# Optimization experiments

Measured on AMD Instinct MI355X. Metric: run time of the kernel, lower is better.

Reference implementation:

```python
import jax, jax.numpy as jnp
import numpy as np

B = 16384          # batch
F = 64             # number of feature columns (tables)
L = 10             # pooled lookups per feature (bag size)
E = 16             # embedding dim
V = 1_000_000      # hashed vocab size (shared table)
D = F * E          # concat width = 1024
EPS = 1e-5


def setup_inputs() -> dict:
    key = jax.random.key(0)
    ks = jax.random.split(key, 9)
    idx = jax.random.randint(ks[0], (B, F, L), 0, V, dtype=jnp.int64)
    # NormalTensorInitializer(var=0.01) -> std 0.1
    emb = jax.random.normal(ks[1], (V, E), dtype=jnp.float32) * 0.1
    W1 = jax.random.normal(ks[2], (D, 1024), dtype=jnp.float32) / np.sqrt(D).astype(np.float32)
    b1 = jnp.zeros((1024,), jnp.float32)
    W2 = jax.random.normal(ks[3], (1024, 512), dtype=jnp.float32) / np.sqrt(1024).astype(np.float32)
    b2 = jnp.zeros((512,), jnp.float32)
    W3 = jax.random.normal(ks[4], (512, 1), dtype=jnp.float32) / np.sqrt(512).astype(np.float32)
    b3 = jnp.zeros((1,), jnp.float32)
    return {"idx": idx, "emb": emb, "W1": W1, "b1": b1,
            "W2": W2, "b2": b2, "W3": W3, "b3": b3}


def reference(idx, emb, W1, b1, W2, b2, W3, b3):
    # EmbeddingSumConcat: gather [B,F,L,E], sum-pool over bag dim, concat features
    pooled = jnp.take(emb, idx, axis=0).sum(axis=2)          # [B, F, E]
    x = pooled.reshape(B, D)                                  # [B, F*E]
    # ms.nn.Normalization: per-feature batch standardization
    mu = x.mean(axis=0, keepdims=True)
    var = x.var(axis=0, keepdims=True)
    x = (x - mu) * jax.lax.rsqrt(var + EPS)
    # Dense tower 1024 -> 1024 -> 512 -> 1, sigmoid
    h = jax.nn.relu(x @ W1 + b1)
    h = jax.nn.relu(h @ W2 + b2)
    out = jax.nn.sigmoid(h @ W3 + b3)                         # [B, 1]
    return out
```

## Files before the change

### kernel.cpp

```cpp
#include <hip/hip_runtime.h>
#include <hip/hip_bf16.h>
#include <math.h>

typedef __attribute__((ext_vector_type(8))) short  short8;
typedef __attribute__((ext_vector_type(4))) float  f32x4;
typedef __attribute__((ext_vector_type(4))) unsigned short u16x4;
typedef __attribute__((ext_vector_type(8))) unsigned short u16x8;

#define BATCH 16384
#define NF    64
#define BAGL  10
#define ED    16
#define DW    1024
#define VOCAB 1000000

static __device__ __forceinline__ unsigned short f2bf(float f) {
    unsigned int u = __builtin_bit_cast(unsigned int, f);
    unsigned int r = (u + 0x7fffu + ((u >> 16) & 1u)) >> 16;
    return (unsigned short)r;
}
static __device__ __forceinline__ float bf2f(unsigned short h) {
    unsigned int u = ((unsigned int)h) << 16;
    return __builtin_bit_cast(float, u);
}

__global__ __launch_bounds__(256) void pool_kernel(const int* __restrict__ idx,
                                                   const float* __restrict__ emb,
                                                   unsigned short* __restrict__ xb) {
    const int gid = blockIdx.x * 256 + threadIdx.x;
    const int bag = gid >> 2;
    const int q   = gid & 3;
    const int* ip = idx + (long long)bag * BAGL;

    int v[BAGL];
#pragma unroll
    for (int l = 0; l < BAGL; ++l) v[l] = ip[l];
    f32x4 e[BAGL];
#pragma unroll
    for (int l = 0; l < BAGL; ++l)
        e[l] = *(const f32x4*)(emb + (((long long)v[l]) << 4) + (q << 2));

    f32x4 s01 = e[0] + e[1], s23 = e[2] + e[3], s45 = e[4] + e[5],
          s67 = e[6] + e[7], s89 = e[8] + e[9];
    f32x4 acc = ((s01 + s23) + (s45 + s67)) + s89;

    u16x4 o;
#pragma unroll
    for (int j = 0; j < 4; ++j) o[j] = f2bf(acc[j]);
    *(u16x4*)(xb + (((long long)bag) << 4) + (q << 2)) = o;
}

__global__ __launch_bounds__(256) void stats_kernel(const unsigned short* __restrict__ xb,
                                                    float* __restrict__ ssum,
                                                    float* __restrict__ ssq) {
    const int t = threadIdx.x;
    const long long r0 = (long long)blockIdx.x * 128;
    float s[4] = {0, 0, 0, 0}, q[4] = {0, 0, 0, 0};
    for (int r = 0; r < 128; ++r) {
        const u16x4 v = *(const u16x4*)(xb + (r0 + r) * DW + t * 4);
#pragma unroll
        for (int j = 0; j < 4; ++j) { float f = bf2f(v[j]); s[j] += f; q[j] += f * f; }
    }
#pragma unroll
    for (int j = 0; j < 4; ++j) {
        atomicAdd(&ssum[t * 4 + j], s[j]);
        atomicAdd(&ssq [t * 4 + j], q[j]);
    }
}

__global__ void finalize_stats(const float* __restrict__ ssum, const float* __restrict__ ssq,
                               float* __restrict__ mean, float* __restrict__ rsig,
                               float* __restrict__ murs) {
    const int c = blockIdx.x * 256 + threadIdx.x;
    const float m = ssum[c] * (1.0f / (float)BATCH);
    const float v = ssq[c] * (1.0f / (float)BATCH) - m * m;
    const float r = rsqrtf(v + 1e-5f);
    mean[c] = m; rsig[c] = r; murs[c] = m * r;
}

template <int SCALE>
__global__ __launch_bounds__(256) void transpose_f32_bf16(const float* __restrict__ src,
                                                          unsigned short* __restrict__ dst,
                                                          int R, int C,
                                                          const float* __restrict__ rs) {
    __shared__ float tile[32][33];
    const int tx = threadIdx.x & 31, ty = threadIdx.x >> 5;
    const int bx = blockIdx.x, by = blockIdx.y;
#pragma unroll
    for (int i = 0; i < 4; ++i) {
        const int r = by * 32 + ty + i * 8, c = bx * 32 + tx;
        float v = src[(long long)r * C + c];
        if (SCALE) v *= rs[r];
        tile[ty + i * 8][tx] = v;
    }
    __syncthreads();
#pragma unroll
    for (int i = 0; i < 4; ++i) {
        const int oc = bx * 32 + ty + i * 8;
        dst[(long long)oc * R + by * 32 + tx] = f2bf(tile[tx][ty + i * 8]);
    }
}

__global__ __launch_bounds__(256) void b1fold_kernel(const float* __restrict__ W1,
                                                     const float* __restrict__ murs,
                                                     float* __restrict__ b1n) {
    const int n = blockIdx.x * 256 + threadIdx.x;
    const int k0 = blockIdx.y * 128;
    float acc = 0.f;
#pragma unroll 4
    for (int k = 0; k < 128; ++k)
        acc += murs[k0 + k] * W1[(long long)(k0 + k) * 1024 + n];
    atomicAdd(&b1n[n], -acc);
}

__global__ __launch_bounds__(512, 2) void gemm1_256(const unsigned short* __restrict__ A,
                                                    const unsigned short* __restrict__ Bt,
                                                    const float* __restrict__ bias,
                                                    const float* __restrict__ bias2,
                                                    unsigned short* __restrict__ C,
                                                    int M, int N, int K) {
    __shared__ __align__(16) unsigned short As[2][256 * 64];
    __shared__ __align__(16) unsigned short Bs[2][256 * 64];
    const int tid = threadIdx.x;
    const int w = tid >> 6, l = tid & 63;
    const int wr = w >> 2, wc = w & 3;
    const int l15 = l & 15, l4 = l >> 4;
    const int blk = blockIdx.x, xcd = blk & 7, jj = blk >> 3;
    const int bm = xcd * 8 + (jj >> 2), bn = jj & 3;

    f32x4 acc[8][4] = {};
    const long long a_base = (long long)bm * 256 * K;
    const long long b_base = (long long)bn * 256 * K;
    const int NT = K >> 6;

#define G1_STAGE(buf, kt)                                                       \
  {                                                                             \
    const int k0s = (kt) * 64;                                                  \
    _Pragma("unroll")                                                           \
    for (int g = 0; g < 4; ++g) {                                               \
      const int cid = g * 512 + tid;                                            \
      const int rr = cid >> 3, pos = cid & 7;                                   \
      const int csrc = (pos ^ (rr & 7)) << 3;                                   \
      __builtin_amdgcn_global_load_lds(                                         \
        (const __attribute__((address_space(1))) void*)(A + a_base + (long long)rr * K + k0s + csrc), \
        (__attribute__((address_space(3))) void*)(&As[buf][cid * 8]), 16, 0, 0);\
      __builtin_amdgcn_global_load_lds(                                         \
        (const __attribute__((address_space(1))) void*)(Bt + b_base + (long long)rr * K + k0s + csrc), \
        (__attribute__((address_space(3))) void*)(&Bs[buf][cid * 8]), 16, 0, 0);\
    }                                                                           \
  }

    G1_STAGE(0, 0)
    G1_STAGE(1, 1)
    asm volatile("s_waitcnt vmcnt(8)" ::: "memory");
    __builtin_amdgcn_sched_barrier(0);
    __builtin_amdgcn_s_barrier();

    for (int t = 0; t < NT; ++t) {
        const unsigned short* Ap = As[t & 1];
        const unsigned short* Bp = Bs[t & 1];
        short8 a[8], b[4];

        {
            const int swz = ((0 * 4 + l4) ^ (l15 & 7)) << 3;
#pragma unroll
            for (int m = 0; m < 8; ++m)
                a[m] = *(const short8*)(Ap + (wr * 128 + m * 16 + l15) * 64 + swz);
#pragma unroll
            for (int n = 0; n < 4; ++n)
                b[n] = *(const short8*)(Bp + (wc * 64 + n * 16 + l15) * 64 + swz);
        }
        asm volatile("s_waitcnt lgkmcnt(0)" ::: "memory");
        __builtin_amdgcn_sched_barrier(0);
        __builtin_amdgcn_s_setprio(1);
#pragma unroll
        for (int m = 0; m < 8; ++m)
#pragma unroll
            for (int n = 0; n < 4; ++n)
                acc[m][n] = __builtin_amdgcn_mfma_f32_16x16x32_bf16(a[m], b[n], acc[m][n], 0, 0, 0);
        __builtin_amdgcn_s_setprio(0);

        {
            const int swz = ((1 * 4 + l4) ^ (l15 & 7)) << 3;
#pragma unroll
            for (int m = 0; m < 8; ++m)
                a[m] = *(const short8*)(Ap + (wr * 128 + m * 16 + l15) * 64 + swz);
#pragma unroll
            for (int n = 0; n < 4; ++n)
                b[n] = *(const short8*)(Bp + (wc * 64 + n * 16 + l15) * 64 + swz);
        }
        asm volatile("s_waitcnt lgkmcnt(0)" ::: "memory");
        __builtin_amdgcn_sched_barrier(0);
        __builtin_amdgcn_s_barrier();
        if (t + 2 < NT) { G1_STAGE((t & 1), t + 2) }
        __builtin_amdgcn_s_setprio(1);
#pragma unroll
        for (int m = 0; m < 8; ++m)
#pragma unroll
            for (int n = 0; n < 4; ++n)
                acc[m][n] = __builtin_amdgcn_mfma_f32_16x16x32_bf16(a[m], b[n], acc[m][n], 0, 0, 0);
        __builtin_amdgcn_s_setprio(0);
        if (t + 1 < NT) {
            if (t + 2 < NT) { asm volatile("s_waitcnt vmcnt(8)" ::: "memory"); }
            else            { asm volatile("s_waitcnt vmcnt(0)" ::: "memory"); }
            __builtin_amdgcn_sched_barrier(0);
            __builtin_amdgcn_s_barrier();
        }
    }
#undef G1_STAGE

#pragma unroll
    for (int m = 0; m < 8; ++m) {
        const int grow_base = bm * 256 + wr * 128 + m * 16 + l4 * 4;
#pragma unroll
        for (int n = 0; n < 4; ++n) {
            const int gcol = bn * 256 + wc * 64 + n * 16 + l15;
            const float bv = bias[gcol] + bias2[gcol];
#pragma unroll
            for (int j2 = 0; j2 < 4; ++j2) {
                float v = fmaxf(acc[m][n][j2] + bv, 0.f);
                C[(long long)(grow_base + j2) * N + gcol] = f2bf(v);
            }
        }
    }
}

#define GEMM_STAGE(dstA, dstB, kt)                                              \
  {                                                                             \
    const int k0s = (kt) * 64;                                                  \
    _Pragma("unroll")                                                           \
    for (int g = 0; g < 4; ++g) {                                               \
      const int cid = g * 256 + tid;                                            \
      const int rr = cid >> 3, pos = cid & 7;                                   \
      const int csrc = (pos ^ (rr & 7)) << 3;                                   \
      __builtin_amdgcn_global_load_lds(                                         \
        (const __attribute__((address_space(1))) void*)(A + a_base + (long long)rr * K + k0s + csrc), \
        (__attribute__((address_space(3))) void*)(&(dstA)[cid * 8]), 16, 0, 0); \
      __builtin_amdgcn_global_load_lds(                                         \
        (const __attribute__((address_space(1))) void*)(Bt + b_base + (long long)rr * K + k0s + csrc), \
        (__attribute__((address_space(3))) void*)(&(dstB)[cid * 8]), 16, 0, 0); \
    }                                                                           \
  }

__global__ __launch_bounds__(256, 2) void gemm2_fused(const unsigned short* __restrict__ A,
                                                      const unsigned short* __restrict__ Bt,
                                                      const float* __restrict__ bias,
                                                      const float* __restrict__ W3,
                                                      float* __restrict__ logits,
                                                      int M, int N, int K, int NBN) {
    __shared__ __align__(16) unsigned short As[2][128 * 64];
    __shared__ __align__(16) unsigned short Bs[2][128 * 64];
    const int tid = threadIdx.x;
    const int w = tid >> 6, l = tid & 63;
    const int wr = w >> 1, wc = w & 1;
    const int l15 = l & 15, l4 = l >> 4;
    const int blk = blockIdx.x, xcd = blk & 7, j = blk >> 3;
    const int bm = xcd * 16 + j / NBN, bn = j % NBN;

    f32x4 acc[4][4] = {};
    const long long a_base = (long long)bm * 128 * K;
    const long long b_base = (long long)bn * 128 * K;
    const int NT = K >> 6;

    GEMM_STAGE(As[0], Bs[0], 0)
    GEMM_STAGE(As[1], Bs[1], 1)
    asm volatile("s_waitcnt vmcnt(8)" ::: "memory");
    __builtin_amdgcn_sched_barrier(0);
    __builtin_amdgcn_s_barrier();
    for (int t = 0; t < NT; ++t) {
        const unsigned short* Ap = As[t & 1];
        const unsigned short* Bp = Bs[t & 1];
        short8 a[2][4], b[2][4];
#pragma unroll
        for (int kk = 0; kk < 2; ++kk) {
            const int swz = ((kk * 4 + l4) ^ (l15 & 7)) << 3;
#pragma unroll
            for (int m = 0; m < 4; ++m)
                a[kk][m] = *(const short8*)(Ap + (wr * 64 + m * 16 + l15) * 64 + swz);
#pragma unroll
            for (int n = 0; n < 4; ++n)
                b[kk][n] = *(const short8*)(Bp + (wc * 64 + n * 16 + l15) * 64 + swz);
        }
        asm volatile("s_waitcnt lgkmcnt(0)" ::: "memory");
        __builtin_amdgcn_sched_barrier(0);
        __builtin_amdgcn_s_barrier();
        if (t + 2 < NT) { GEMM_STAGE(As[t & 1], Bs[t & 1], t + 2) }
        __builtin_amdgcn_s_setprio(1);
#pragma unroll
        for (int kk = 0; kk < 2; ++kk)
#pragma unroll
            for (int m = 0; m < 4; ++m)
#pragma unroll
                for (int n = 0; n < 4; ++n)
                    acc[m][n] = __builtin_amdgcn_mfma_f32_16x16x32_bf16(a[kk][m], b[kk][n], acc[m][n], 0, 0, 0);
        __builtin_amdgcn_s_setprio(0);
        if (t + 1 < NT) {
            if (t + 2 < NT) { asm volatile("s_waitcnt vmcnt(8)" ::: "memory"); }
            else            { asm volatile("s_waitcnt vmcnt(0)" ::: "memory"); }
            __builtin_amdgcn_sched_barrier(0);
            __builtin_amdgcn_s_barrier();
        }
    }

#pragma unroll
    for (int m = 0; m < 4; ++m) {
        float part[4] = {0.f, 0.f, 0.f, 0.f};
#pragma unroll
        for (int n = 0; n < 4; ++n) {
            const int gcol = bn * 128 + wc * 64 + n * 16 + l15;
            const float bv = bias[gcol];
            const float w3 = W3[gcol];
#pragma unroll
            for (int j2 = 0; j2 < 4; ++j2) {
                float v = fmaxf(acc[m][n][j2] + bv, 0.f);
                part[j2] += v * w3;
            }
        }
#pragma unroll
        for (int off = 1; off < 16; off <<= 1)
#pragma unroll
            for (int j2 = 0; j2 < 4; ++j2) part[j2] += __shfl_xor(part[j2], off, 64);
        if (l15 == 0) {
            const int grow = bm * 128 + wr * 64 + m * 16 + l4 * 4;
#pragma unroll
            for (int j2 = 0; j2 < 4; ++j2) atomicAdd(&logits[grow + j2], part[j2]);
        }
    }
}

__global__ __launch_bounds__(256) void sigmoid_kernel(const float* __restrict__ logits,
                                                      const float* __restrict__ b3,
                                                      float* __restrict__ out) {
    const int i = blockIdx.x * 256 + threadIdx.x;
    out[i] = 1.0f / (1.0f + expf(-(logits[i] + b3[0])));
}

extern "C" void kernel_launch(void* const* d_in, const int* in_sizes, int n_in,
                              void* d_out, int out_size, void* d_ws, size_t ws_size,
                              hipStream_t stream) {
    const int*   idx = (const int*)d_in[0];
    const float* emb = (const float*)d_in[1];
    const float* W1  = (const float*)d_in[2];
    const float* b1  = (const float*)d_in[3];
    const float* W2  = (const float*)d_in[4];
    const float* b2  = (const float*)d_in[5];
    const float* W3  = (const float*)d_in[6];
    const float* b3  = (const float*)d_in[7];
    float* out = (float*)d_out;

    char* ws = (char*)d_ws;
    unsigned short* xb   = (unsigned short*)ws; ws += (size_t)BATCH * DW * 2;
    unsigned short* h1   = (unsigned short*)ws; ws += (size_t)BATCH * DW * 2;
    unsigned short* w1t  = (unsigned short*)ws; ws += (size_t)1024 * 1024 * 2;
    unsigned short* w2t  = (unsigned short*)ws; ws += (size_t)512 * 1024 * 2;
    float* ssum   = (float*)ws; ws += 4096;
    float* ssq    = (float*)ws; ws += 4096;
    float* b1n    = (float*)ws; ws += 4096;
    float* logits = (float*)ws; ws += (size_t)BATCH * 4;
    float* mean   = (float*)ws; ws += 4096;
    float* rsig   = (float*)ws; ws += 4096;
    float* murs   = (float*)ws; ws += 4096;

    hipMemsetAsync(ssum, 0, 4096 * 3 + (size_t)BATCH * 4, stream);

    pool_kernel<<<(BATCH * NF * 4) / 256, 256, 0, stream>>>(idx, emb, xb);
    stats_kernel<<<BATCH / 128, 256, 0, stream>>>(xb, ssum, ssq);
    finalize_stats<<<4, 256, 0, stream>>>(ssum, ssq, mean, rsig, murs);

    transpose_f32_bf16<1><<<dim3(32, 32), 256, 0, stream>>>(W1, w1t, 1024, 1024, rsig);
    b1fold_kernel<<<dim3(4, 8), 256, 0, stream>>>(W1, murs, b1n);
    transpose_f32_bf16<0><<<dim3(16, 32), 256, 0, stream>>>(W2, w2t, 1024, 512, nullptr);

    gemm1_256<<<(BATCH / 256) * (1024 / 256), 512, 0, stream>>>(
        xb, w1t, b1, b1n, h1, BATCH, 1024, 1024);
    gemm2_fused<<<(BATCH / 128) * (512 / 128), 256, 0, stream>>>(
        h1, w2t, b2, W3, logits, BATCH, 512, 1024, 512 / 128);

    sigmoid_kernel<<<BATCH / 256, 256, 0, stream>>>(logits, b3, out);
}
```

Before: 296.9 us.

## Fuse stats finalize into weight prep, merge transposes, asm embedding loads

Drops the finalize_stats kernel by computing rsqrt of the variance inline in the weight transpose and bias-fold kernels. Merges the W1 and W2 transposes into one launch using a z-dimension. Doubles the number of stats blocks so each covers fewer rows. Rewrites the embedding gather with inline-asm global_load_dwordx4 using 32-bit offsets against a scalar base, which removes 64-bit address math but assumes every offset fits in 32 bits.

```diff
diff --git a/kernel.cpp b/kernel.cpp
--- a/kernel.cpp
+++ b/kernel.cpp
@@ -31,17 +31,24 @@
     const int bag = gid >> 2;
     const int q   = gid & 3;
     const int* ip = idx + (long long)bag * BAGL;
-
-    int v[BAGL];
-#pragma unroll
-    for (int l = 0; l < BAGL; ++l) v[l] = ip[l];
-    f32x4 e[BAGL];
-#pragma unroll
-    for (int l = 0; l < BAGL; ++l)
-        e[l] = *(const f32x4*)(emb + (((long long)v[l]) << 4) + (q << 2));
-
-    f32x4 s01 = e[0] + e[1], s23 = e[2] + e[3], s45 = e[4] + e[5],
-          s67 = e[6] + e[7], s89 = e[8] + e[9];
+    const unsigned qb = (unsigned)(q << 4);
+
+    unsigned o0 = ((unsigned)ip[0] << 6) + qb, o1 = ((unsigned)ip[1] << 6) + qb,
+             o2 = ((unsigned)ip[2] << 6) + qb, o3 = ((unsigned)ip[3] << 6) + qb,
+             o4 = ((unsigned)ip[4] << 6) + qb, o5 = ((unsigned)ip[5] << 6) + qb,
+             o6 = ((unsigned)ip[6] << 6) + qb, o7 = ((unsigned)ip[7] << 6) + qb,
+             o8 = ((unsigned)ip[8] << 6) + qb, o9 = ((unsigned)ip[9] << 6) + qb;
+
+    f32x4 e0, e1, e2, e3, e4, e5, e6, e7, e8, e9;
+#define GLD(e, o) asm volatile("global_load_dwordx4 %0, %1, %2" \
+                               : "=v"(e) : "v"(o), "s"(emb))
+    GLD(e0, o0); GLD(e1, o1); GLD(e2, o2); GLD(e3, o3); GLD(e4, o4);
+    GLD(e5, o5); GLD(e6, o6); GLD(e7, o7); GLD(e8, o8); GLD(e9, o9);
+#undef GLD
+    asm volatile("s_waitcnt vmcnt(0)" ::: "memory");
+    __builtin_amdgcn_sched_barrier(0);
+
+    f32x4 s01 = e0 + e1, s23 = e2 + e3, s45 = e4 + e5, s67 = e6 + e7, s89 = e8 + e9;
     f32x4 acc = ((s01 + s23) + (s45 + s67)) + s89;
 
     u16x4 o;
@@ -54,9 +61,9 @@
                                                     float* __restrict__ ssum,
                                                     float* __restrict__ ssq) {
     const int t = threadIdx.x;
-    const long long r0 = (long long)blockIdx.x * 128;
+    const long long r0 = (long long)blockIdx.x * 64;
     float s[4] = {0, 0, 0, 0}, q[4] = {0, 0, 0, 0};
-    for (int r = 0; r < 128; ++r) {
+    for (int r = 0; r < 64; ++r) {
         const u16x4 v = *(const u16x4*)(xb + (r0 + r) * DW + t * 4);
 #pragma unroll
         for (int j = 0; j < 4; ++j) { float f = bf2f(v[j]); s[j] += f; q[j] += f * f; }
@@ -68,48 +75,57 @@
     }
 }
 
-__global__ void finalize_stats(const float* __restrict__ ssum, const float* __restrict__ ssq,
-                               float* __restrict__ mean, float* __restrict__ rsig,
-                               float* __restrict__ murs) {
-    const int c = blockIdx.x * 256 + threadIdx.x;
+static __device__ __forceinline__ float rsig_of(const float* ssum, const float* ssq, int c) {
     const float m = ssum[c] * (1.0f / (float)BATCH);
     const float v = ssq[c] * (1.0f / (float)BATCH) - m * m;
-    const float r = rsqrtf(v + 1e-5f);
-    mean[c] = m; rsig[c] = r; murs[c] = m * r;
-}
-
-template <int SCALE>
-__global__ __launch_bounds__(256) void transpose_f32_bf16(const float* __restrict__ src,
-                                                          unsigned short* __restrict__ dst,
-                                                          int R, int C,
-                                                          const float* __restrict__ rs) {
+    return rsqrtf(v + 1e-5f);
+}
+
+__global__ __launch_bounds__(256) void prep_weights(const float* __restrict__ W1,
+                                                    const float* __restrict__ W2,
+                                                    const float* __restrict__ ssum,
+                                                    const float* __restrict__ ssq,
+                                                    unsigned short* __restrict__ w1t,
+                                                    unsigned short* __restrict__ w2t) {
+    const int z = blockIdx.z;
+    const int bx = blockIdx.x, by = blockIdx.y;
+    if (z == 1 && bx >= 16) return;
     __shared__ float tile[32][33];
     const int tx = threadIdx.x & 31, ty = threadIdx.x >> 5;
-    const int bx = blockIdx.x, by = blockIdx.y;
+    const float* src = z ? W2 : W1;
+    unsigned short* dst = z ? w2t : w1t;
+    const int C = z ? 512 : 1024;
 #pragma unroll
     for (int i = 0; i < 4; ++i) {
         const int r = by * 32 + ty + i * 8, c = bx * 32 + tx;
         float v = src[(long long)r * C + c];
-        if (SCALE) v *= rs[r];
+        if (!z) v *= rsig_of(ssum, ssq, r);
         tile[ty + i * 8][tx] = v;
     }
     __syncthreads();
 #pragma unroll
     for (int i = 0; i < 4; ++i) {
         const int oc = bx * 32 + ty + i * 8;
-        dst[(long long)oc * R + by * 32 + tx] = f2bf(tile[tx][ty + i * 8]);
+        dst[(long long)oc * 1024 + by * 32 + tx] = f2bf(tile[tx][ty + i * 8]);
     }
 }
 
 __global__ __launch_bounds__(256) void b1fold_kernel(const float* __restrict__ W1,
-                                                     const float* __restrict__ murs,
+                                                     const float* __restrict__ ssum,
+                                                     const float* __restrict__ ssq,
                                                      float* __restrict__ b1n) {
+    __shared__ float mu_s[128];
     const int n = blockIdx.x * 256 + threadIdx.x;
     const int k0 = blockIdx.y * 128;
+    if (threadIdx.x < 128) {
+        const int k = k0 + threadIdx.x;
+        mu_s[threadIdx.x] = ssum[k] * (1.0f / (float)BATCH) * rsig_of(ssum, ssq, k);
+    }
+    __syncthreads();
     float acc = 0.f;
 #pragma unroll 4
     for (int k = 0; k < 128; ++k)
-        acc += murs[k0 + k] * W1[(long long)(k0 + k) * 1024 + n];
+        acc += mu_s[k] * W1[(long long)(k0 + k) * 1024 + n];
     atomicAdd(&b1n[n], -acc);
 }
 
@@ -162,7 +178,7 @@
         short8 a[8], b[4];
 
         {
-            const int swz = ((0 * 4 + l4) ^ (l15 & 7)) << 3;
+            const int swz = (l4 ^ (l15 & 7)) << 3;
 #pragma unroll
             for (int m = 0; m < 8; ++m)
                 a[m] = *(const short8*)(Ap + (wr * 128 + m * 16 + l15) * 64 + swz);
@@ -181,7 +197,7 @@
         __builtin_amdgcn_s_setprio(0);
 
         {
-            const int swz = ((1 * 4 + l4) ^ (l15 & 7)) << 3;
+            const int swz = ((4 + l4) ^ (l15 & 7)) << 3;
 #pragma unroll
             for (int m = 0; m < 8; ++m)
                 a[m] = *(const short8*)(Ap + (wr * 128 + m * 16 + l15) * 64 + swz);
@@ -357,19 +373,14 @@
     float* ssq    = (float*)ws; ws += 4096;
     float* b1n    = (float*)ws; ws += 4096;
     float* logits = (float*)ws; ws += (size_t)BATCH * 4;
-    float* mean   = (float*)ws; ws += 4096;
-    float* rsig   = (float*)ws; ws += 4096;
-    float* murs   = (float*)ws; ws += 4096;
 
     hipMemsetAsync(ssum, 0, 4096 * 3 + (size_t)BATCH * 4, stream);
 
     pool_kernel<<<(BATCH * NF * 4) / 256, 256, 0, stream>>>(idx, emb, xb);
-    stats_kernel<<<BATCH / 128, 256, 0, stream>>>(xb, ssum, ssq);
-    finalize_stats<<<4, 256, 0, stream>>>(ssum, ssq, mean, rsig, murs);
-
-    transpose_f32_bf16<1><<<dim3(32, 32), 256, 0, stream>>>(W1, w1t, 1024, 1024, rsig);
-    b1fold_kernel<<<dim3(4, 8), 256, 0, stream>>>(W1, murs, b1n);
-    transpose_f32_bf16<0><<<dim3(16, 32), 256, 0, stream>>>(W2, w2t, 1024, 512, nullptr);
+    stats_kernel<<<BATCH / 64, 256, 0, stream>>>(xb, ssum, ssq);
+
+    prep_weights<<<dim3(32, 32, 2), 256, 0, stream>>>(W1, W2, ssum, ssq, w1t, w2t);
+    b1fold_kernel<<<dim3(4, 8), 256, 0, stream>>>(W1, ssum, ssq, b1n);
 
     gemm1_256<<<(BATCH / 256) * (1024 / 256), 512, 0, stream>>>(
         xb, w1t, b1, b1n, h1, BATCH, 1024, 1024);
```

Measured after the change: 303.9 us. +2.3%, slower.
